# Kernel optimization log

Measured on AMD Instinct MI355X. Metric: run time of the kernel, lower is better.

## Reference

```python
import jax, jax.numpy as jnp
import numpy as np

N_NODES = 50000
N_EDGES = 800000
IN_DIM = 128
HID = 64
HEADS = 4
EMB = 128
N_GRAPHS = 64
NEG_SLOPE = 0.2


def setup_inputs() -> dict:
    key = jax.random.key(0)
    ks = jax.random.split(key, 12)
    x = jax.random.normal(ks[0], (N_NODES, IN_DIM), dtype=jnp.float32)
    edge_index = jax.random.randint(ks[1], (2, N_EDGES), 0, N_NODES, dtype=jnp.int64)
    edge_weight = jax.random.uniform(ks[2], (N_EDGES,), dtype=jnp.float32)
    batch_vec = jnp.sort(jax.random.randint(ks[3], (N_NODES,), 0, N_GRAPHS, dtype=jnp.int64))
    # GATConv layer 1: in_dim -> hid, heads=4, concat
    s1 = 1.0 / np.sqrt(IN_DIM)
    W1 = jax.random.uniform(ks[4], (IN_DIM, HEADS * HID), jnp.float32, -s1, s1)
    a_src1 = jax.random.uniform(ks[5], (HEADS, HID), jnp.float32, -s1, s1)
    a_dst1 = jax.random.uniform(ks[6], (HEADS, HID), jnp.float32, -s1, s1)
    b1 = jnp.zeros((HEADS * HID,), jnp.float32)
    # GATConv layer 2: heads*hid -> emb, heads=1, mean
    s2 = 1.0 / np.sqrt(HEADS * HID)
    W2 = jax.random.uniform(ks[7], (HEADS * HID, EMB), jnp.float32, -s2, s2)
    a_src2 = jax.random.uniform(ks[8], (1, EMB), jnp.float32, -s2, s2)
    a_dst2 = jax.random.uniform(ks[9], (1, EMB), jnp.float32, -s2, s2)
    b2 = jnp.zeros((EMB,), jnp.float32)
    return {"x": x, "edge_index": edge_index, "edge_weight": edge_weight,
            "batch_vec": batch_vec, "W1": W1, "a_src1": a_src1, "a_dst1": a_dst1,
            "b1": b1, "W2": W2, "a_src2": a_src2, "a_dst2": a_dst2, "b2": b2}


def gat_conv(x, src, dst, W, a_src, a_dst, bias, heads, out_dim, concat):
    N = x.shape[0]
    h = (x @ W).reshape(N, heads, out_dim)                 # [N,H,C]
    alpha_s = jnp.sum(h * a_src, axis=-1)                  # [N,H]
    alpha_d = jnp.sum(h * a_dst, axis=-1)                  # [N,H]
    e = jax.nn.leaky_relu(alpha_s[src] + alpha_d[dst], NEG_SLOPE)  # [E,H]
    # segment softmax over edges grouped by destination node
    m = jax.ops.segment_max(e, dst, num_segments=N)        # [N,H]
    w = jnp.exp(e - m[dst])
    z = jax.ops.segment_sum(w, dst, num_segments=N)
    alpha = w / z[dst]                                     # [E,H]
    msg = h[src] * alpha[:, :, None]                       # [E,H,C]
    out = jax.ops.segment_sum(msg, dst, num_segments=N)    # [N,H,C]
    out = out.reshape(N, heads * out_dim) if concat else out.mean(axis=1)
    return out + bias


def reference(x, edge_index, edge_weight, batch_vec, W1, a_src1, a_dst1, b1, W2, a_src2, a_dst2, b2):
    N = x.shape[0]
    loop = jnp.arange(N, dtype=edge_index.dtype)
    src = jnp.concatenate([edge_index[0], loop])           # add_self_loops=True
    dst = jnp.concatenate([edge_index[1], loop])
    h = gat_conv(x, src, dst, W1, a_src1, a_dst1, b1, HEADS, HID, True)
    h = jax.nn.elu(h)                                      # dropout = identity (eval mode)
    h = gat_conv(h, src, dst, W2, a_src2, a_dst2, b2, 1, EMB, False)
    h = jax.nn.elu(h)
    # global mean pool over batch_vec
    sums = jax.ops.segment_sum(h, batch_vec, num_segments=N_GRAPHS)
    cnts = jax.ops.segment_sum(jnp.ones((N,), h.dtype), batch_vec, num_segments=N_GRAPHS)
    return sums / jnp.maximum(cnts, 1.0)[:, None]
```

## Files before the change

### kernel.cpp

```cpp
#include <hip/hip_runtime.h>
#include <hip/hip_bf16.h>
#include <cstddef>

constexpr int N_NODES = 50000;
constexpr int N_EDGES = 800000;
constexpr int IN_DIM  = 128;
constexpr int HID     = 64;
constexpr int HEADS   = 4;
constexpr int F1      = HEADS * HID;
constexpr int EMB     = 128;
constexpr int N_GRAPHS = 64;

constexpr int DEG_BLOCKS   = (N_EDGES + 255) / 256;
constexpr int SCAN_BLOCKS  = (N_NODES + 255) / 256;
constexpr int W1_FRAG = 4 * 4 * 64 * 8;
constexpr int LDSB = 264;
constexpr int AXS  = HEADS * IN_DIM + 8;
constexpr int NBUCK    = (N_NODES + 255) / 256;
constexpr int P1_CHUNK = 8192;
constexpr int P1_BLOCKS = (N_EDGES + P1_CHUNK - 1) / P1_CHUNK;
constexpr int AS_BLOCKS = N_NODES / 16;
constexpr int AGG12_BLOCKS = N_NODES / 16;
static_assert(N_NODES % 16 == 0, "16-row tiling assumes exact fit");

typedef __bf16 bf16x8 __attribute__((ext_vector_type(8)));
typedef __bf16 bf16x2 __attribute__((ext_vector_type(2)));
typedef float  f32x4  __attribute__((ext_vector_type(4)));
typedef float  f32x2  __attribute__((ext_vector_type(2)));

__device__ __forceinline__ float lrelu(float x) { return x > 0.f ? x : 0.2f * x; }
__device__ __forceinline__ float eluf(float x)  { return x > 0.f ? x : expm1f(x); }
__device__ __forceinline__ f32x2 s2(float s)    { return (f32x2){s, s}; }

__device__ __forceinline__ void pack_frag(const float* __restrict__ B,
                                          __bf16* __restrict__ hi,
                                          __bf16* __restrict__ lo,
                                          int pblk, int NT, int KK, int ld, int col0) {
    const int gid = pblk * 256 + threadIdx.x;
    if (gid >= NT * KK * 64) return;
    const int lane = gid & 63;
    const int rem  = gid >> 6;
    const int kk   = rem % KK;
    const int t    = rem / KK;
    const int n    = col0 + t * 16 + (lane & 15);
    const int k0   = kk * 32 + (lane >> 4) * 8;
#pragma unroll
    for (int j = 0; j < 8; j++) {
        const float v = B[(size_t)(k0 + j) * ld + n];
        const __bf16 h = (__bf16)v;
        hi[(size_t)gid * 8 + j] = h;
        lo[(size_t)gid * 8 + j] = (__bf16)(v - (float)h);
    }
}

__global__ __launch_bounds__(256) void prep_kernel(const int* __restrict__ ei,
                                                   int* __restrict__ deg,
                                                   const float* __restrict__ W1,
                                                   __bf16* __restrict__ B1h,
                                                   __bf16* __restrict__ B1l,
                                                   const float* __restrict__ W2,
                                                   __bf16* __restrict__ B2h,
                                                   __bf16* __restrict__ B2l,
                                                   const float* __restrict__ as1v,
                                                   const float* __restrict__ ad1v,
                                                   float* __restrict__ wst) {
    const int b = blockIdx.x;
    if (b < DEG_BLOCKS) {
        const int e = b * 256 + threadIdx.x;
        if (e < N_EDGES) atomicAdd(&deg[ei[N_EDGES + e]], 1);
        return;
    }
    const int pb = b - DEG_BLOCKS;
    if (pb < 16) {
        const int head = pb >> 2;
        pack_frag(W1, B1h + head * W1_FRAG, B1l + head * W1_FRAG,
                  pb & 3, 4, 4, F1, head * HID);
        return;
    }
    if (pb < 32) {
        pack_frag(W2, B2h, B2l, pb - 16, 8, 8, EMB, 0);
        return;
    }
    const int gid = (pb - 32) * 256 + threadIdx.x;
    const int o = gid >> 7, c = gid & 127;
    const int h = o & 3;
    const float* av = (o < 4) ? as1v : ad1v;
    float s = 0.f;
#pragma unroll 8
    for (int k = 0; k < HID; k++)
        s += W1[(size_t)c * F1 + h * HID + k] * av[h * HID + k];
    wst[o * IN_DIM + c] = s;
}

__global__ __launch_bounds__(256) void scanA_kernel(const int* __restrict__ deg,
                                                    int* __restrict__ off,
                                                    int* __restrict__ partial, int N) {
    __shared__ int sm[256];
    const int t = threadIdx.x;
    const int i = blockIdx.x * 256 + t;
    const int v = (i < N) ? deg[i] : 0;
    sm[t] = v;
    __syncthreads();
    int val = v;
#pragma unroll
    for (int o = 1; o < 256; o <<= 1) {
        const int add = (t >= o) ? sm[t - o] : 0;
        __syncthreads();
        val += add;
        sm[t] = val;
        __syncthreads();
    }
    if (i < N) off[i] = val - v;
    if (t == 255) partial[blockIdx.x] = val;
}

__global__ __launch_bounds__(256) void scanB_kernel(int* __restrict__ partial,
                                                    int* __restrict__ off_last) {
    __shared__ int sm[256];
    const int t = threadIdx.x;
    const int v = (t < SCAN_BLOCKS) ? partial[t] : 0;
    sm[t] = v;
    __syncthreads();
    int val = v;
#pragma unroll
    for (int o = 1; o < 256; o <<= 1) {
        const int add = (t >= o) ? sm[t - o] : 0;
        __syncthreads();
        val += add;
        sm[t] = val;
        __syncthreads();
    }
    if (t < SCAN_BLOCKS) partial[t] = val - v;
    if (t == SCAN_BLOCKS - 1) *off_last = val;
}

__global__ __launch_bounds__(256) void scanC_kernel(int* __restrict__ off,
                                                    const int* __restrict__ partial,
                                                    int* __restrict__ cur,
                                                    int* __restrict__ gcur, int N) {
    const int i = blockIdx.x * 256 + threadIdx.x;
    if (i < N) {
        const int o = off[i] + partial[blockIdx.x];
        off[i] = o;
        cur[i] = 0;
        if ((i & 255) == 0) gcur[i >> 8] = o;
    }
}

__global__ __launch_bounds__(256) void as_scatter_kernel(
        const float* __restrict__ x, const float* __restrict__ wst,
        float* __restrict__ as_out, float* __restrict__ ad_out,
        __bf16* __restrict__ xb,
        const int* __restrict__ ei, int* __restrict__ gcur,
        unsigned* __restrict__ stage) {
    const int tid = threadIdx.x;
    if (blockIdx.x < AS_BLOCKS) {
        const int n   = blockIdx.x * 16 + (tid >> 4);
        const int l16 = tid & 15;
        const int d8  = l16 * 8;
        const float4 xa = *(const float4*)&x[(size_t)n * IN_DIM + d8];
        const float4 xc = *(const float4*)&x[(size_t)n * IN_DIM + d8 + 4];
        bf16x8 bw;
        bw[0] = (__bf16)xa.x; bw[1] = (__bf16)xa.y;
        bw[2] = (__bf16)xa.z; bw[3] = (__bf16)xa.w;
        bw[4] = (__bf16)xc.x; bw[5] = (__bf16)xc.y;
        bw[6] = (__bf16)xc.z; bw[7] = (__bf16)xc.w;
        *(bf16x8*)&xb[(size_t)n * IN_DIM + d8] = bw;
        float p[8];
#pragma unroll
        for (int o = 0; o < 8; o++) {
            const float4 wa = *(const float4*)&wst[o * IN_DIM + d8];
            const float4 wb = *(const float4*)&wst[o * IN_DIM + d8 + 4];
            p[o] = xa.x * wa.x + xa.y * wa.y + xa.z * wa.z + xa.w * wa.w
                 + xc.x * wb.x + xc.y * wb.y + xc.z * wb.z + xc.w * wb.w;
        }
#pragma unroll
        for (int off = 1; off < 16; off <<= 1) {
#pragma unroll
            for (int o = 0; o < 8; o++) p[o] += __shfl_xor(p[o], off);
        }
        if (l16 == 0) {
            *(float4*)&as_out[n * HEADS] = (float4){p[0], p[1], p[2], p[3]};
            *(float4*)&ad_out[n * HEADS] = (float4){p[4], p[5], p[6], p[7]};
        }
        return;
    }
    __shared__ int lhist[NBUCK];
    __shared__ int lbase[NBUCK];
    const int e0 = (blockIdx.x - AS_BLOCKS) * P1_CHUNK;
    for (int b = tid; b < NBUCK; b += 256) lhist[b] = 0;
    __syncthreads();
    for (int i = 0; i < P1_CHUNK / 256; i++) {
        const int e = e0 + i * 256 + tid;
        if (e < N_EDGES) atomicAdd(&lhist[ei[N_EDGES + e] >> 8], 1);
    }
    __syncthreads();
    for (int b = tid; b < NBUCK; b += 256) {
        const int c = lhist[b];
        lbase[b] = c ? atomicAdd(&gcur[b], c) : 0;
    }
    __syncthreads();
    for (int b = tid; b < NBUCK; b += 256) lhist[b] = 0;
    __syncthreads();
    for (int i = 0; i < P1_CHUNK / 256; i++) {
        const int e = e0 + i * 256 + tid;
        if (e < N_EDGES) {
            const int s = ei[e], d = ei[N_EDGES + e];
            const int bk = d >> 8;
            const int r  = atomicAdd(&lhist[bk], 1);
            stage[lbase[bk] + r] = (unsigned)s | ((unsigned)d << 16);
        }
    }
}

__global__ __launch_bounds__(256) void w1s_kernel(const unsigned* __restrict__ stage,
                                                  const int* __restrict__ off,
                                                  int* __restrict__ cur,
                                                  const float* __restrict__ as1,
                                                  const float* __restrict__ ad1,
                                                  int* __restrict__ col,
                                                  float4* __restrict__ w4, int E) {
    const int i = blockIdx.x * 256 + threadIdx.x;
    if (i >= E) return;
    const unsigned p = stage[i];
    const int s = (int)(p & 0xFFFFu);
    const int d = (int)(p >> 16);
    const float4 a = *(const float4*)&as1[s * HEADS];
    const float4 b = *(const float4*)&ad1[d * HEADS];
    const int pos = off[d] + atomicAdd(&cur[d], 1);
    float4 o;
    o.x = __expf(lrelu(a.x + b.x));
    o.y = __expf(lrelu(a.y + b.y));
    o.z = __expf(lrelu(a.z + b.z));
    o.w = __expf(lrelu(a.w + b.w));
    col[pos] = s;
    w4[pos] = o;
}

__global__ __launch_bounds__(256, 4) void agg_gemm12_kernel(
        const int* __restrict__ off, const int* __restrict__ col,
        const float4* __restrict__ w4, const __bf16* __restrict__ xb,
        const float* __restrict__ as1, const float* __restrict__ ad1,
        const __bf16* __restrict__ B1h, const __bf16* __restrict__ B1l,
        const float* __restrict__ b1,
        const __bf16* __restrict__ B2h, const __bf16* __restrict__ B2l,
        const float* __restrict__ avs, const float* __restrict__ avd,
        __bf16* __restrict__ g2b, float* __restrict__ as_out,
        float* __restrict__ ad_out, int M) {
    __shared__ __bf16 axh[16 * AXS];
    __shared__ __bf16 axl[16 * AXS];
    __shared__ float pps[4][16], pdd[4][16];
    __bf16* const smh = axh;
    __bf16* const sml = axl;
    const int tid  = threadIdx.x;
    const int wave = tid >> 6, lane = tid & 63;
    const int quad = lane >> 4, l16 = lane & 15;
    const int row0 = blockIdx.x * 16;

    {
        const int ln = wave * 4 + quad;
        const int w  = row0 + ln;
        const int d8 = l16 * 8;
        float acc[HEADS][8];
        float z[HEADS];
        {
            const float4 asv = *(const float4*)&as1[w * HEADS];
            const float4 adv = *(const float4*)&ad1[w * HEADS];
            const float ws0 = __expf(lrelu(asv.x + adv.x));
            const float ws1 = __expf(lrelu(asv.y + adv.y));
            const float ws2 = __expf(lrelu(asv.z + adv.z));
            const float ws3 = __expf(lrelu(asv.w + adv.w));
            const bf16x8 xv = *(const bf16x8*)&xb[(size_t)w * IN_DIM + d8];
#pragma unroll
            for (int d = 0; d < 8; d++) {
                const float xf = (float)xv[d];
                acc[0][d] = ws0 * xf; acc[1][d] = ws1 * xf;
                acc[2][d] = ws2 * xf; acc[3][d] = ws3 * xf;
            }
            z[0] = ws0; z[1] = ws1; z[2] = ws2; z[3] = ws3;
        }
        const int jb = off[w], je = off[w + 1];
        int j = jb;
        for (; j + 3 < je; j += 4) {
            int    s[4];
            float4 ww[4];
            bf16x8 bv[4];
#pragma unroll
            for (int u = 0; u < 4; u++) s[u] = col[j + u];
#pragma unroll
            for (int u = 0; u < 4; u++) ww[u] = w4[j + u];
#pragma unroll
            for (int u = 0; u < 4; u++)
                bv[u] = *(const bf16x8*)&xb[(size_t)s[u] * IN_DIM + d8];
#pragma unroll
            for (int u = 0; u < 4; u++) {
#pragma unroll
                for (int d = 0; d < 8; d++) {
                    const float xf = (float)bv[u][d];
                    acc[0][d] += ww[u].x * xf;
                    acc[1][d] += ww[u].y * xf;
                    acc[2][d] += ww[u].z * xf;
                    acc[3][d] += ww[u].w * xf;
                }
                z[0] += ww[u].x; z[1] += ww[u].y;
                z[2] += ww[u].z; z[3] += ww[u].w;
            }
        }
        for (; j < je; j++) {
            const int s0 = col[j];
            const float4 w0 = w4[j];
            const bf16x8 b0 = *(const bf16x8*)&xb[(size_t)s0 * IN_DIM + d8];
#pragma unroll
            for (int d = 0; d < 8; d++) {
                const float xf = (float)b0[d];
                acc[0][d] += w0.x * xf; acc[1][d] += w0.y * xf;
                acc[2][d] += w0.z * xf; acc[3][d] += w0.w * xf;
            }
            z[0] += w0.x; z[1] += w0.y; z[2] += w0.z; z[3] += w0.w;
        }
#pragma unroll
        for (int h = 0; h < HEADS; h++) {
            const float inv = 1.f / z[h];
            bf16x8 hv, lv;
#pragma unroll
            for (int d = 0; d < 8; d++) {
                const float v = acc[h][d] * inv;
                const __bf16 hh = (__bf16)v;
                hv[d] = hh;
                lv[d] = (__bf16)(v - (float)hh);
            }
            const int o = ln * AXS + h * IN_DIM + d8;
            *(bf16x8*)&axh[o] = hv;
            *(bf16x8*)&axl[o] = lv;
        }
    }
    __syncthreads();

    {
        bf16x8 ahv[4], alv[4];
        const int abase = l16 * AXS + wave * IN_DIM;
#pragma unroll
        for (int kk = 0; kk < 4; kk++) {
            const int k0 = kk * 32 + quad * 8;
            ahv[kk] = *(const bf16x8*)&axh[abase + k0];
            alv[kk] = *(const bf16x8*)&axl[abase + k0];
        }
        __syncthreads();

        f32x4 acc1[4];
#pragma unroll
        for (int t = 0; t < 4; t++) acc1[t] = (f32x4){0.f, 0.f, 0.f, 0.f};
#pragma unroll
        for (int kk = 0; kk < 4; kk++) {
#pragma unroll
            for (int t = 0; t < 4; t++) {
                const size_t bi = (size_t)wave * W1_FRAG +
                                  ((size_t)(t * 4 + kk) * 64 + lane) * 8;
                bf16x8 bhv = *(const bf16x8*)&B1h[bi];
                bf16x8 blv = *(const bf16x8*)&B1l[bi];
                acc1[t] = __builtin_amdgcn_mfma_f32_16x16x32_bf16(ahv[kk], bhv, acc1[t], 0, 0, 0);
                acc1[t] = __builtin_amdgcn_mfma_f32_16x16x32_bf16(alv[kk], bhv, acc1[t], 0, 0, 0);
                acc1[t] = __builtin_amdgcn_mfma_f32_16x16x32_bf16(ahv[kk], blv, acc1[t], 0, 0, 0);
            }
        }
#pragma unroll
        for (int t = 0; t < 4; t++) {
            const int c = wave * 64 + t * 16 + l16;
            const float bb = b1[c];
#pragma unroll
            for (int r = 0; r < 4; r++) {
                const float v = eluf(acc1[t][r] + bb);
                const __bf16 hh = (__bf16)v;
                smh[(quad * 4 + r) * LDSB + c] = hh;
                sml[(quad * 4 + r) * LDSB + c] = (__bf16)(v - (float)hh);
            }
        }
    }
    __syncthreads();

    f32x4 acc2[2];
#pragma unroll
    for (int t = 0; t < 2; t++) acc2[t] = (f32x4){0.f, 0.f, 0.f, 0.f};
    const int arow = l16 * LDSB;
#pragma unroll
    for (int kk = 0; kk < 8; kk++) {
        const int k0 = kk * 32 + quad * 8;
        bf16x8 ah = *(const bf16x8*)&smh[arow + k0];
        bf16x8 al = *(const bf16x8*)&sml[arow + k0];
#pragma unroll
        for (int tt = 0; tt < 2; tt++) {
            const int t = wave * 2 + tt;
            const size_t bi = ((size_t)(t * 8 + kk) * 64 + lane) * 8;
            bf16x8 bhv = *(const bf16x8*)&B2h[bi];
            bf16x8 blv = *(const bf16x8*)&B2l[bi];
            acc2[tt] = __builtin_amdgcn_mfma_f32_16x16x32_bf16(ah, bhv, acc2[tt], 0, 0, 0);
            acc2[tt] = __builtin_amdgcn_mfma_f32_16x16x32_bf16(al, bhv, acc2[tt], 0, 0, 0);
            acc2[tt] = __builtin_amdgcn_mfma_f32_16x16x32_bf16(ah, blv, acc2[tt], 0, 0, 0);
        }
    }

    const int rowS = row0 + quad * 4;
#pragma unroll
    for (int tt = 0; tt < 2; tt++) {
        const int t = wave * 2 + tt;
#pragma unroll
        for (int r = 0; r < 4; r++) {
            const int rr = rowS + r;
            if (rr < M) g2b[(size_t)rr * EMB + t * 16 + l16] = (__bf16)acc2[tt][r];
        }
    }
#pragma unroll
    for (int r = 0; r < 4; r++) {
        float ps = 0.f, pd = 0.f;
#pragma unroll
        for (int tt = 0; tt < 2; tt++) {
            const int c = (wave * 2 + tt) * 16 + l16;
            ps += acc2[tt][r] * avs[c];
            pd += acc2[tt][r] * avd[c];
        }
#pragma unroll
        for (int o = 1; o < 16; o <<= 1) {
            ps += __shfl_xor(ps, o);
            pd += __shfl_xor(pd, o);
        }
        if (l16 == 0) {
            pps[wave][quad * 4 + r] = ps;
            pdd[wave][quad * 4 + r] = pd;
        }
    }
    __syncthreads();
    if (tid < 16) {
        const int rr = row0 + tid;
        if (rr < M) {
            as_out[rr] = pps[0][tid] + pps[1][tid] + pps[2][tid] + pps[3][tid];
            ad_out[rr] = pdd[0][tid] + pdd[1][tid] + pdd[2][tid] + pdd[3][tid];
        }
    }
}

__global__ __launch_bounds__(256) void agg2_kernel(const int* __restrict__ off,
                                                   const int* __restrict__ col,
                                                   const float* __restrict__ as2,
                                                   const float* __restrict__ ad2,
                                                   const __bf16* __restrict__ g2b,
                                                   __bf16* __restrict__ out2, int N) {
    const int w  = blockIdx.x * 16 + (threadIdx.x >> 4);
    const int d8 = (threadIdx.x & 15) * 8;
    const float ad2w = ad2[w];
    f32x2 acc[4];
    float z;
    {
        const float wt = __expf(lrelu(as2[w] + ad2w));
        const bf16x8 hv = *(const bf16x8*)&g2b[(size_t)w * EMB + d8];
#pragma unroll
        for (int p = 0; p < 4; p++) {
            const f32x2 xf = {(float)hv[2 * p], (float)hv[2 * p + 1]};
            acc[p] = s2(wt) * xf;
        }
        z = wt;
    }
    const int jb = off[w], je = off[w + 1];
    int j = jb;
    for (; j + 3 < je; j += 4) {
        int s[4];
#pragma unroll
        for (int u = 0; u < 4; u++) s[u] = col[j + u];
        float av[4];
#pragma unroll
        for (int u = 0; u < 4; u++) av[u] = as2[s[u]];
        bf16x8 bv[4];
#pragma unroll
        for (int u = 0; u < 4; u++)
            bv[u] = *(const bf16x8*)&g2b[(size_t)s[u] * EMB + d8];
#pragma unroll
        for (int u = 0; u < 4; u++) {
            const float wt = __expf(lrelu(av[u] + ad2w));
#pragma unroll
            for (int p = 0; p < 4; p++) {
                const f32x2 xf = {(float)bv[u][2 * p], (float)bv[u][2 * p + 1]};
                acc[p] += s2(wt) * xf;
            }
            z += wt;
        }
    }
    for (; j < je; j++) {
        const int s0 = col[j];
        const float wt = __expf(lrelu(as2[s0] + ad2w));
        const bf16x8 b0 = *(const bf16x8*)&g2b[(size_t)s0 * EMB + d8];
#pragma unroll
        for (int p = 0; p < 4; p++) {
            const f32x2 xf = {(float)b0[2 * p], (float)b0[2 * p + 1]};
            acc[p] += s2(wt) * xf;
        }
        z += wt;
    }
    const float inv = 1.f / z;
    bf16x8 ov;
#pragma unroll
    for (int p = 0; p < 4; p++) {
        ov[2 * p]     = (__bf16)(acc[p][0] * inv);
        ov[2 * p + 1] = (__bf16)(acc[p][1] * inv);
    }
    *(bf16x8*)&out2[(size_t)w * EMB + d8] = ov;
}

__global__ __launch_bounds__(128) void pool_kernel(const __bf16* __restrict__ out2,
                                                   const float* __restrict__ b2,
                                                   const int* __restrict__ batch,
                                                   float* __restrict__ pool,
                                                   float* __restrict__ cnt, int N) {
    const int c = threadIdx.x;
    const int n0 = blockIdx.x * 64;
    const int nend = min(n0 + 64, N);
    const float bias = b2[c];
    float acc = 0.f, cacc = 0.f;
    int curg = batch[n0];
    for (int n = n0; n < nend; n++) {
        const int g = batch[n];
        if (g != curg) {
            atomicAdd(&pool[curg * EMB + c], acc);
            if (c == 0) atomicAdd(&cnt[curg], cacc);
            acc = 0.f; cacc = 0.f; curg = g;
        }
        float v = (float)out2[(size_t)n * EMB + c] + bias;
        v = v > 0.f ? v : expm1f(v);
        acc += v;
        cacc += 1.f;
    }
    atomicAdd(&pool[curg * EMB + c], acc);
    if (c == 0) atomicAdd(&cnt[curg], cacc);
}

__global__ __launch_bounds__(256) void div_kernel(const float* __restrict__ pool,
                                                  const float* __restrict__ cnt,
                                                  float* __restrict__ out) {
    const int i = blockIdx.x * 256 + threadIdx.x;
    out[i] = pool[i] / fmaxf(cnt[i >> 7], 1.f);
}

extern "C" void kernel_launch(void* const* d_in, const int* in_sizes, int n_in,
                              void* d_out, int out_size, void* d_ws, size_t ws_size,
                              hipStream_t stream) {
    const float* x      = (const float*)d_in[0];
    const int*   ei     = (const int*)d_in[1];
    const int*   batch  = (const int*)d_in[3];
    const float* W1     = (const float*)d_in[4];
    const float* a_src1 = (const float*)d_in[5];
    const float* a_dst1 = (const float*)d_in[6];
    const float* b1     = (const float*)d_in[7];
    const float* W2     = (const float*)d_in[8];
    const float* a_src2 = (const float*)d_in[9];
    const float* a_dst2 = (const float*)d_in[10];
    const float* b2     = (const float*)d_in[11];
    float* out = (float*)d_out;

    const int N = N_NODES, E = N_EDGES;

    size_t cur_off = 0;
    auto carve = [&](size_t bytes) {
        size_t o = cur_off;
        cur_off = (cur_off + bytes + 255) & ~(size_t)255;
        return (char*)d_ws + o;
    };
    int* deg     = (int*)carve((size_t)N * 4);
    float* pool  = (float*)carve((size_t)N_GRAPHS * EMB * 4);
    float* cnt   = (float*)carve((size_t)N_GRAPHS * 4);
    const size_t zero_bytes = cur_off;
    int* curp    = (int*)carve((size_t)N * 4);
    int* partial = (int*)carve((size_t)SCAN_BLOCKS * 4);
    int* gcur    = (int*)carve((size_t)NBUCK * 4);
    unsigned* stage = (unsigned*)carve((size_t)E * 4);
    float* wst   = (float*)carve((size_t)8 * IN_DIM * 4);
    __bf16* B1h  = (__bf16*)carve((size_t)HEADS * W1_FRAG * 2);
    __bf16* B1l  = (__bf16*)carve((size_t)HEADS * W1_FRAG * 2);
    __bf16* B2h  = (__bf16*)carve((size_t)F1 * EMB * 2);
    __bf16* B2l  = (__bf16*)carve((size_t)F1 * EMB * 2);
    __bf16* xb   = (__bf16*)carve((size_t)N * IN_DIM * 2);
    int* off     = (int*)carve((size_t)(N + 1) * 4);
    int* col     = (int*)carve((size_t)E * 4);
    float4* w4   = (float4*)carve((size_t)E * 16);
    __bf16* g2b  = (__bf16*)carve((size_t)N * EMB * 2);
    __bf16* out2 = (__bf16*)carve((size_t)N * EMB * 2);
    float* as1   = (float*)carve((size_t)N * HEADS * 4);
    float* ad1   = (float*)carve((size_t)N * HEADS * 4);
    float* as2   = (float*)carve((size_t)N * 4);
    float* ad2   = (float*)carve((size_t)N * 4);

    hipMemsetAsync(d_ws, 0, zero_bytes, stream);

    prep_kernel<<<DEG_BLOCKS + 36, 256, 0, stream>>>(
        ei, deg, W1, B1h, B1l, W2, B2h, B2l, a_src1, a_dst1, wst);

    scanA_kernel<<<SCAN_BLOCKS, 256, 0, stream>>>(deg, off, partial, N);
    scanB_kernel<<<1, 256, 0, stream>>>(partial, &off[N]);
    scanC_kernel<<<SCAN_BLOCKS, 256, 0, stream>>>(off, partial, curp, gcur, N);

    as_scatter_kernel<<<AS_BLOCKS + P1_BLOCKS, 256, 0, stream>>>(
        x, wst, as1, ad1, xb, ei, gcur, stage);

    w1s_kernel<<<DEG_BLOCKS, 256, 0, stream>>>(stage, off, curp, as1, ad1, col, w4, E);

    agg_gemm12_kernel<<<AGG12_BLOCKS, 256, 0, stream>>>(off, col, w4, xb, as1, ad1,
                                                        B1h, B1l, b1, B2h, B2l,
                                                        a_src2, a_dst2,
                                                        g2b, as2, ad2, N);

    agg2_kernel<<<AGG12_BLOCKS, 256, 0, stream>>>(off, col, as2, ad2, g2b, out2, N);

    pool_kernel<<<(N + 63) / 64, 128, 0, stream>>>(out2, b2, batch, pool, cnt, N);
    div_kernel<<<(N_GRAPHS * EMB) / 256, 256, 0, stream>>>(pool, cnt, out);
}
```

Measured before the change: 321.3 us.

## Replace per-node degree scan with bucket histogram and per-bucket CSR distribution

The CSR build now counts edges per 256-node bucket using shared-memory histograms, replacing the per-node global atomic degree count. It then runs a single small scan over the buckets, and a distribute kernel builds per-node offsets and scatters edges within each bucket using LDS atomics. This removes the three-kernel node scan and the global per-node atomics from the old w1s pass. In exchange, the stage array is read twice per bucket and each bucket is handled by a single block, so a skewed bucket would limit that pass. The P1 chunk size is reduced to give more blocks.

After: 281.4 us. 1.14x faster.

```diff
diff --git a/kernel.cpp b/kernel.cpp
--- a/kernel.cpp
+++ b/kernel.cpp
@@ -11,13 +11,11 @@
 constexpr int EMB     = 128;
 constexpr int N_GRAPHS = 64;
 
-constexpr int DEG_BLOCKS   = (N_EDGES + 255) / 256;
-constexpr int SCAN_BLOCKS  = (N_NODES + 255) / 256;
 constexpr int W1_FRAG = 4 * 4 * 64 * 8;
 constexpr int LDSB = 264;
 constexpr int AXS  = HEADS * IN_DIM + 8;
 constexpr int NBUCK    = (N_NODES + 255) / 256;
-constexpr int P1_CHUNK = 8192;
+constexpr int P1_CHUNK = 2048;
 constexpr int P1_BLOCKS = (N_EDGES + P1_CHUNK - 1) / P1_CHUNK;
 constexpr int AS_BLOCKS = N_NODES / 16;
 constexpr int AGG12_BLOCKS = N_NODES / 16;
@@ -54,7 +52,7 @@
 }
 
 __global__ __launch_bounds__(256) void prep_kernel(const int* __restrict__ ei,
-                                                   int* __restrict__ deg,
+                                                   int* __restrict__ bcnt,
                                                    const float* __restrict__ W1,
                                                    __bf16* __restrict__ B1h,
                                                    __bf16* __restrict__ B1l,
@@ -65,12 +63,25 @@
                                                    const float* __restrict__ ad1v,
                                                    float* __restrict__ wst) {
     const int b = blockIdx.x;
-    if (b < DEG_BLOCKS) {
-        const int e = b * 256 + threadIdx.x;
-        if (e < N_EDGES) atomicAdd(&deg[ei[N_EDGES + e]], 1);
+    if (b < P1_BLOCKS) {
+        __shared__ int lh[NBUCK];
+        const int tid = threadIdx.x;
+        for (int i = tid; i < NBUCK; i += 256) lh[i] = 0;
+        __syncthreads();
+        const int e0 = b * P1_CHUNK;
+#pragma unroll
+        for (int i = 0; i < P1_CHUNK / 256; i++) {
+            const int e = e0 + i * 256 + tid;
+            if (e < N_EDGES) atomicAdd(&lh[ei[N_EDGES + e] >> 8], 1);
+        }
+        __syncthreads();
+        for (int i = tid; i < NBUCK; i += 256) {
+            const int c = lh[i];
+            if (c) atomicAdd(&bcnt[i], c);
+        }
         return;
     }
-    const int pb = b - DEG_BLOCKS;
+    const int pb = b - P1_BLOCKS;
     if (pb < 16) {
         const int head = pb >> 2;
         pack_frag(W1, B1h + head * W1_FRAG, B1l + head * W1_FRAG,
@@ -92,13 +103,12 @@
     wst[o * IN_DIM + c] = s;
 }
 
-__global__ __launch_bounds__(256) void scanA_kernel(const int* __restrict__ deg,
-                                                    int* __restrict__ off,
-                                                    int* __restrict__ partial, int N) {
+__global__ __launch_bounds__(256) void scan196_kernel(const int* __restrict__ bcnt,
+                                                      int* __restrict__ gbase,
+                                                      int* __restrict__ gcur) {
     __shared__ int sm[256];
     const int t = threadIdx.x;
-    const int i = blockIdx.x * 256 + t;
-    const int v = (i < N) ? deg[i] : 0;
+    const int v = (t < NBUCK) ? bcnt[t] : 0;
     sm[t] = v;
     __syncthreads();
     int val = v;
@@ -110,44 +120,11 @@
         sm[t] = val;
         __syncthreads();
     }
-    if (i < N) off[i] = val - v;
-    if (t == 255) partial[blockIdx.x] = val;
-}
-
-__global__ __launch_bounds__(256) void scanB_kernel(int* __restrict__ partial,
-                                                    int* __restrict__ off_last) {
-    __shared__ int sm[256];
-    const int t = threadIdx.x;
-    const int v = (t < SCAN_BLOCKS) ? partial[t] : 0;
-    sm[t] = v;
-    __syncthreads();
-    int val = v;
-#pragma unroll
-    for (int o = 1; o < 256; o <<= 1) {
-        const int add = (t >= o) ? sm[t - o] : 0;
-        __syncthreads();
-        val += add;
-        sm[t] = val;
-        __syncthreads();
-    }
-    if (t < SCAN_BLOCKS) partial[t] = val - v;
-    if (t == SCAN_BLOCKS - 1) *off_last = val;
-}
-
-__global__ __launch_bounds__(256) void scanC_kernel(int* __restrict__ off,
-                                                    const int* __restrict__ partial,
-                                                    int* __restrict__ cur,
-                                                    int* __restrict__ gcur, int N) {
-    const int i = blockIdx.x * 256 + threadIdx.x;
-    if (i < N) {
-        const int o = off[i] + partial[blockIdx.x];
-        off[i] = o;
-        cur[i] = 0;
-        if ((i & 255) == 0) gcur[i >> 8] = o;
-    }
-}
-
-__global__ __launch_bounds__(256) void as_scatter_kernel(
+    if (t < NBUCK) { gbase[t] = val - v; gcur[t] = val - v; }
+    if (t == NBUCK - 1) gbase[NBUCK] = val;
+}
+
+__global__ __launch_bounds__(256) void proj_append_kernel(
         const float* __restrict__ x, const float* __restrict__ wst,
         float* __restrict__ as_out, float* __restrict__ ad_out,
         __bf16* __restrict__ xb,
@@ -190,6 +167,7 @@
     const int e0 = (blockIdx.x - AS_BLOCKS) * P1_CHUNK;
     for (int b = tid; b < NBUCK; b += 256) lhist[b] = 0;
     __syncthreads();
+#pragma unroll
     for (int i = 0; i < P1_CHUNK / 256; i++) {
         const int e = e0 + i * 256 + tid;
         if (e < N_EDGES) atomicAdd(&lhist[ei[N_EDGES + e] >> 8], 1);
@@ -202,6 +180,7 @@
     __syncthreads();
     for (int b = tid; b < NBUCK; b += 256) lhist[b] = 0;
     __syncthreads();
+#pragma unroll
     for (int i = 0; i < P1_CHUNK / 256; i++) {
         const int e = e0 + i * 256 + tid;
         if (e < N_EDGES) {
@@ -213,32 +192,61 @@
     }
 }
 
-__global__ __launch_bounds__(256) void w1s_kernel(const unsigned* __restrict__ stage,
-                                                  const int* __restrict__ off,
-                                                  int* __restrict__ cur,
-                                                  const float* __restrict__ as1,
-                                                  const float* __restrict__ ad1,
-                                                  int* __restrict__ col,
-                                                  float4* __restrict__ w4, int E) {
-    const int i = blockIdx.x * 256 + threadIdx.x;
-    if (i >= E) return;
-    const unsigned p = stage[i];
-    const int s = (int)(p & 0xFFFFu);
-    const int d = (int)(p >> 16);
-    const float4 a = *(const float4*)&as1[s * HEADS];
-    const float4 b = *(const float4*)&ad1[d * HEADS];
-    const int pos = off[d] + atomicAdd(&cur[d], 1);
-    float4 o;
-    o.x = __expf(lrelu(a.x + b.x));
-    o.y = __expf(lrelu(a.y + b.y));
-    o.z = __expf(lrelu(a.z + b.z));
-    o.w = __expf(lrelu(a.w + b.w));
-    col[pos] = s;
-    w4[pos] = o;
+__global__ __launch_bounds__(256) void distribute_kernel(
+        const unsigned* __restrict__ stage, const int* __restrict__ gbase,
+        const float* __restrict__ as1, const float* __restrict__ ad1,
+        int* __restrict__ off, int* __restrict__ offE,
+        int* __restrict__ col, float4* __restrict__ w4, int N) {
+    __shared__ int lcnt[256];
+    __shared__ int sm[256];
+    __shared__ int lcur[256];
+    const int t = threadIdx.x;
+    const int b = blockIdx.x;
+    const int wb = gbase[b], we = gbase[b + 1];
+    lcnt[t] = 0;
+    __syncthreads();
+    for (int j = wb + t; j < we; j += 256)
+        atomicAdd(&lcnt[(stage[j] >> 16) & 255], 1);
+    __syncthreads();
+    const int v = lcnt[t];
+    sm[t] = v;
+    __syncthreads();
+    int val = v;
+#pragma unroll
+    for (int o = 1; o < 256; o <<= 1) {
+        const int add = (t >= o) ? sm[t - o] : 0;
+        __syncthreads();
+        val += add;
+        sm[t] = val;
+        __syncthreads();
+    }
+    const int node = b * 256 + t;
+    if (node < N) {
+        off[node]  = wb + val - v;
+        offE[node] = wb + val;
+    }
+    lcur[t] = wb + val - v;
+    __syncthreads();
+    for (int j = wb + t; j < we; j += 256) {
+        const unsigned p = stage[j];
+        const int s = (int)(p & 0xFFFFu);
+        const int d = (int)(p >> 16);
+        const int pos = atomicAdd(&lcur[d & 255], 1);
+        const float4 a  = *(const float4*)&as1[s * HEADS];
+        const float4 bb = *(const float4*)&ad1[d * HEADS];
+        float4 o;
+        o.x = __expf(lrelu(a.x + bb.x));
+        o.y = __expf(lrelu(a.y + bb.y));
+        o.z = __expf(lrelu(a.z + bb.z));
+        o.w = __expf(lrelu(a.w + bb.w));
+        col[pos] = s;
+        w4[pos] = o;
+    }
 }
 
 __global__ __launch_bounds__(256, 4) void agg_gemm12_kernel(
-        const int* __restrict__ off, const int* __restrict__ col,
+        const int* __restrict__ off, const int* __restrict__ offE,
+        const int* __restrict__ col,
         const float4* __restrict__ w4, const __bf16* __restrict__ xb,
         const float* __restrict__ as1, const float* __restrict__ ad1,
         const __bf16* __restrict__ B1h, const __bf16* __restrict__ B1l,
@@ -279,7 +287,7 @@
             }
             z[0] = ws0; z[1] = ws1; z[2] = ws2; z[3] = ws3;
         }
-        const int jb = off[w], je = off[w + 1];
+        const int jb = off[w], je = offE[w];
         int j = jb;
         for (; j + 3 < je; j += 4) {
             int    s[4];
@@ -439,6 +447,7 @@
 }
 
 __global__ __launch_bounds__(256) void agg2_kernel(const int* __restrict__ off,
+                                                   const int* __restrict__ offE,
                                                    const int* __restrict__ col,
                                                    const float* __restrict__ as2,
                                                    const float* __restrict__ ad2,
@@ -459,7 +468,7 @@
         }
         z = wt;
     }
-    const int jb = off[w], je = off[w + 1];
+    const int jb = off[w], je = offE[w];
     int j = jb;
     for (; j + 3 < je; j += 4) {
         int s[4];
@@ -562,12 +571,11 @@
         cur_off = (cur_off + bytes + 255) & ~(size_t)255;
         return (char*)d_ws + o;
     };
-    int* deg     = (int*)carve((size_t)N * 4);
     float* pool  = (float*)carve((size_t)N_GRAPHS * EMB * 4);
     float* cnt   = (float*)carve((size_t)N_GRAPHS * 4);
+    int* bcnt    = (int*)carve((size_t)NBUCK * 4);
     const size_t zero_bytes = cur_off;
-    int* curp    = (int*)carve((size_t)N * 4);
-    int* partial = (int*)carve((size_t)SCAN_BLOCKS * 4);
+    int* gbase   = (int*)carve((size_t)(NBUCK + 1) * 4);
     int* gcur    = (int*)carve((size_t)NBUCK * 4);
     unsigned* stage = (unsigned*)carve((size_t)E * 4);
     float* wst   = (float*)carve((size_t)8 * IN_DIM * 4);
@@ -576,7 +584,8 @@
     __bf16* B2h  = (__bf16*)carve((size_t)F1 * EMB * 2);
     __bf16* B2l  = (__bf16*)carve((size_t)F1 * EMB * 2);
     __bf16* xb   = (__bf16*)carve((size_t)N * IN_DIM * 2);
-    int* off     = (int*)carve((size_t)(N + 1) * 4);
+    int* off     = (int*)carve((size_t)N * 4);
+    int* offE    = (int*)carve((size_t)N * 4);
     int* col     = (int*)carve((size_t)E * 4);
     float4* w4   = (float4*)carve((size_t)E * 16);
     __bf16* g2b  = (__bf16*)carve((size_t)N * EMB * 2);
@@ -588,24 +597,24 @@
 
     hipMemsetAsync(d_ws, 0, zero_bytes, stream);
 
-    prep_kernel<<<DEG_BLOCKS + 36, 256, 0, stream>>>(
-        ei, deg, W1, B1h, B1l, W2, B2h, B2l, a_src1, a_dst1, wst);
-
-    scanA_kernel<<<SCAN_BLOCKS, 256, 0, stream>>>(deg, off, partial, N);
-    scanB_kernel<<<1, 256, 0, stream>>>(partial, &off[N]);
-    scanC_kernel<<<SCAN_BLOCKS, 256, 0, stream>>>(off, partial, curp, gcur, N);
-
-    as_scatter_kernel<<<AS_BLOCKS + P1_BLOCKS, 256, 0, stream>>>(
+    prep_kernel<<<P1_BLOCKS + 36, 256, 0, stream>>>(
+        ei, bcnt, W1, B1h, B1l, W2, B2h, B2l, a_src1, a_dst1, wst);
+
+    scan196_kernel<<<1, 256, 0, stream>>>(bcnt, gbase, gcur);
+
+    proj_append_kernel<<<AS_BLOCKS + P1_BLOCKS, 256, 0, stream>>>(
         x, wst, as1, ad1, xb, ei, gcur, stage);
 
-    w1s_kernel<<<DEG_BLOCKS, 256, 0, stream>>>(stage, off, curp, as1, ad1, col, w4, E);
-
-    agg_gemm12_kernel<<<AGG12_BLOCKS, 256, 0, stream>>>(off, col, w4, xb, as1, ad1,
-                                                        B1h, B1l, b1, B2h, B2l,
-                                                        a_src2, a_dst2,
+    distribute_kernel<<<NBUCK, 256, 0, stream>>>(stage, gbase, as1, ad1,
+                                                 off, offE, col, w4, N);
+
+    agg_gemm12_kernel<<<AGG12_BLOCKS, 256, 0, stream>>>(off, offE, col, w4, xb,
+                                                        as1, ad1, B1h, B1l, b1,
+                                                        B2h, B2l, a_src2, a_dst2,
                                                         g2b, as2, ad2, N);
 
-    agg2_kernel<<<AGG12_BLOCKS, 256, 0, stream>>>(off, col, as2, ad2, g2b, out2, N);
+    agg2_kernel<<<AGG12_BLOCKS, 256, 0, stream>>>(off, offE, col, as2, ad2,
+                                                  g2b, out2, N);
 
     pool_kernel<<<(N + 63) / 64, 128, 0, stream>>>(out2, b2, batch, pool, cnt, N);
     div_kernel<<<(N_GRAPHS * EMB) / 256, 256, 0, stream>>>(pool, cnt, out);
```
